# Kernel tuning notes

Measured on AMD Instinct MI355X. Metric: run time of the kernel, lower is better.

Reference implementation:

```python
import jax, jax.numpy as jnp
import numpy as np

N = 8192
IN_F = 256
OUT_F = 64
ALPHA = 0.2
NEG_INF = -9e15


def setup_inputs() -> dict:
    key = jax.random.key(0)
    k1, k2, k3, k4 = jax.random.split(key, 4)
    h = jax.random.normal(k1, (N, IN_F), dtype=jnp.float32)
    W = jax.random.normal(k2, (IN_F, OUT_F), dtype=jnp.float32) * (1.414 / np.sqrt(IN_F))
    a = jax.random.normal(k3, (2 * OUT_F, 1), dtype=jnp.float32) * (1.414 / np.sqrt(2 * OUT_F))
    adj = jax.random.randint(k4, (N, N), 0, 2, dtype=jnp.int32)
    return {"h": h, "W": W, "a": a, "adj": adj}


def reference(h, W, a, adj):
    # Wh: [N, F]
    Wh = h @ W
    # Decompose concat-based attention: e_ij = LeakyReLU(Wh_i . a[:F] + Wh_j . a[F:])
    a1, a2 = a[:OUT_F], a[OUT_F:]
    src = Wh @ a1              # [N, 1] contribution of row i
    dst = Wh @ a2              # [N, 1] contribution of col j
    e = jax.nn.leaky_relu(src + dst.T, negative_slope=ALPHA)  # [N, N]
    e = jnp.where(adj > 0, e, NEG_INF)
    attention = jax.nn.softmax(e, axis=1)
    # dropout is identity in eval mode
    h_prime = attention @ Wh   # [N, F]
    return h_prime
```

## Files before the change

### kernel.cpp

```cpp
#include <hip/hip_runtime.h>

#define NROWS 8192
#define NSPLIT 16
#define JT (NROWS / NSPLIT)
#define NITER (JT / 64)
#define L2E 1.4426950408889634f

typedef __attribute__((ext_vector_type(4))) float f32x4;
typedef __attribute__((ext_vector_type(8))) __bf16 bf16x8;
typedef __attribute__((ext_vector_type(4))) unsigned int u32x4;

__device__ __forceinline__ unsigned short f2bf(float x) {
  unsigned u = __float_as_uint(x);
  u += 0x7fffu + ((u >> 16) & 1u);
  return (unsigned short)(u >> 16);
}

__global__ __launch_bounds__(256) void k_prep(
    const float* __restrict__ h, const float* __restrict__ W,
    const float* __restrict__ a, unsigned short* __restrict__ WhB,
    float* __restrict__ src, float* __restrict__ dst) {
  int i = blockIdx.x * 4 + (threadIdx.x >> 6);
  int lane = threadIdx.x & 63;
  const float* hrow = h + (size_t)i * 256;
  float s = 0.f;
#pragma unroll 4
  for (int k = 0; k < 256; k += 4) {
    float4 hv = *(const float4*)(hrow + k);
    s = fmaf(hv.x, W[(k + 0) * 64 + lane], s);
    s = fmaf(hv.y, W[(k + 1) * 64 + lane], s);
    s = fmaf(hv.z, W[(k + 2) * 64 + lane], s);
    s = fmaf(hv.w, W[(k + 3) * 64 + lane], s);
  }
  int nt = lane >> 4, c = lane & 15;
  int gi = (i >> 3) & 3, e = i & 7;
  int idx = ((((i >> 5) * 4 + nt) * 64) + c + 16 * gi) * 8 + e;
  WhB[idx] = f2bf(s);
  float v1 = s * a[lane];
  float v2 = s * a[64 + lane];
#pragma unroll
  for (int d = 32; d; d >>= 1) {
    v1 += __shfl_xor(v1, d);
    v2 += __shfl_xor(v2, d);
  }
  if (lane == 0) {
    src[i] = v1 * L2E;
    dst[i] = v2 * L2E;
  }
}

__global__ __launch_bounds__(256) void k_dmax(
    const float* __restrict__ dst, float* __restrict__ dmax) {
  __shared__ float red[4];
  float v = -INFINITY;
  for (int i = threadIdx.x; i < NROWS; i += 256) v = fmaxf(v, dst[i]);
#pragma unroll
  for (int d = 32; d; d >>= 1) v = fmaxf(v, __shfl_xor(v, d));
  if ((threadIdx.x & 63) == 0) red[threadIdx.x >> 6] = v;
  __syncthreads();
  if (threadIdx.x == 0)
    *dmax = fmaxf(fmaxf(red[0], red[1]), fmaxf(red[2], red[3]));
}

__global__ __launch_bounds__(256, 8) void k_attn(
    const int* __restrict__ adj, const unsigned short* __restrict__ WhB,
    const float* __restrict__ src, const float* __restrict__ dst,
    const float* __restrict__ dmax,
    float* __restrict__ pl, float* __restrict__ pacc) {
  __shared__ float ldst[JT];
  int task = blockIdx.x * 4 + (threadIdx.x >> 6);
  int sp = task >> 9;
  int mt = task & 511;
  int lane = threadIdx.x & 63;
  int r = lane & 15;
  int g = lane >> 4;
  int row0 = mt * 16;
  int jbase = sp * JT;

  for (int k = threadIdx.x; k < JT; k += 256) ldst[k] = dst[jbase + k];
  __syncthreads();

  unsigned long long mk0 = 0, mk1 = 0;
  {
    const int* abase = adj + (size_t)row0 * NROWS + jbase + lane;
#pragma unroll
    for (int rr = 0; rr < 16; ++rr) {
      const int* rp = abase + (size_t)rr * NROWS;
#pragma unroll
      for (int ch = 0; ch < 8; ++ch) {
        int v = rp[ch * 64];
        unsigned long long bal = __ballot(v > 0);
        const int holder = ((ch & 3) << 4) + rr;
        if (ch < 4) mk0 = (lane == holder) ? bal : mk0;
        else        mk1 = (lane == holder) ? bal : mk1;
      }
    }
  }

  float srcr = src[row0 + r];
  float vB = srcr + *dmax;
  float Mi = fmaxf(vB, 0.2f * vB);

  float lrow = 0.f;
  f32x4 acc[4] = {f32x4{0.f, 0.f, 0.f, 0.f}, f32x4{0.f, 0.f, 0.f, 0.f},
                  f32x4{0.f, 0.f, 0.f, 0.f}, f32x4{0.f, 0.f, 0.f, 0.f}};
  const bf16x8* Bfr = (const bf16x8*)WhB;

#define PE(P, BIT, DD)                    \
  {                                       \
    float v_ = srcr + (DD);               \
    v_ = fmaxf(v_, 0.2f * v_);            \
    float e_ = exp2f(v_ - Mi);            \
    (P) = (BIT) ? e_ : 0.f;               \
  }
#define HALF(JC, BITS, DOFF)                                               \
  {                                                                        \
    const bf16x8* bp = Bfr + (size_t)(JC) * 256 + lane;                    \
    bf16x8 b0 = bp[0];                                                     \
    bf16x8 b1 = bp[64];                                                    \
    bf16x8 b2 = bp[128];                                                   \
    bf16x8 b3 = bp[192];                                                   \
    const float4* dlp = (const float4*)(ldst + (DOFF));                    \
    float4 dA = dlp[0];                                                    \
    float4 dB = dlp[1];                                                    \
    unsigned bt_ = (BITS);                                                 \
    float p0, p1, p2, p3, p4, p5, p6, p7;                                  \
    PE(p0, bt_ & 1u, dA.x)   PE(p1, bt_ & 2u, dA.y)                        \
    PE(p2, bt_ & 4u, dA.z)   PE(p3, bt_ & 8u, dA.w)                        \
    PE(p4, bt_ & 16u, dB.x)  PE(p5, bt_ & 32u, dB.y)                       \
    PE(p6, bt_ & 64u, dB.z)  PE(p7, bt_ & 128u, dB.w)                      \
    lrow += ((p0 + p1) + (p2 + p3)) + ((p4 + p5) + (p6 + p7));             \
    unsigned q0, q1, q2, q3;                                               \
    asm("v_cvt_pk_bf16_f32 %0, %1, %2" : "=v"(q0) : "v"(p0), "v"(p1));     \
    asm("v_cvt_pk_bf16_f32 %0, %1, %2" : "=v"(q1) : "v"(p2), "v"(p3));     \
    asm("v_cvt_pk_bf16_f32 %0, %1, %2" : "=v"(q2) : "v"(p4), "v"(p5));     \
    asm("v_cvt_pk_bf16_f32 %0, %1, %2" : "=v"(q3) : "v"(p6), "v"(p7));     \
    u32x4 qv = {q0, q1, q2, q3};                                           \
    bf16x8 Af = __builtin_bit_cast(bf16x8, qv);                            \
    __builtin_amdgcn_s_setprio(1);                                         \
    acc[0] = __builtin_amdgcn_mfma_f32_16x16x32_bf16(Af, b0, acc[0], 0, 0, 0); \
    acc[1] = __builtin_amdgcn_mfma_f32_16x16x32_bf16(Af, b1, acc[1], 0, 0, 0); \
    acc[2] = __builtin_amdgcn_mfma_f32_16x16x32_bf16(Af, b2, acc[2], 0, 0, 0); \
    acc[3] = __builtin_amdgcn_mfma_f32_16x16x32_bf16(Af, b3, acc[3], 0, 0, 0); \
    __builtin_amdgcn_s_setprio(0);                                         \
  }

#pragma unroll 1
  for (int it = 0; it < NITER; ++it) {
    unsigned long long msrc = (it < 4) ? mk0 : mk1;
    unsigned long long pw = __shfl(msrc, ((it & 3) << 4) + r);
    int jc = sp * 16 + 2 * it;
    HALF(jc, (unsigned)(pw >> (8 * g)), it * 64 + 8 * g)
    HALF(jc + 1, (unsigned)(pw >> (32 + 8 * g)), it * 64 + 32 + 8 * g)
  }
#undef HALF
#undef PE

  lrow += __shfl_xor(lrow, 16);
  lrow += __shfl_xor(lrow, 32);
  if (lane < 16) pl[sp * NROWS + row0 + lane] = lrow;
#pragma unroll
  for (int nt = 0; nt < 4; nt++)
#pragma unroll
    for (int q2 = 0; q2 < 4; q2++)
      pacc[((size_t)sp * NROWS + row0 + 4 * g + q2) * 64 + nt * 16 + r] = acc[nt][q2];
}

__global__ __launch_bounds__(256) void k_comb(
    const float* __restrict__ pl, const float* __restrict__ pacc,
    float* __restrict__ out) {
  int t = blockIdx.x * 256 + threadIdx.x;
  int row = t >> 6, f = t & 63;
  float L = 0.f, o = 0.f;
#pragma unroll
  for (int s2 = 0; s2 < NSPLIT; s2++) {
    L += pl[s2 * NROWS + row];
    o += pacc[((size_t)s2 * NROWS + row) * 64 + f];
  }
  out[t] = o / L;
}

extern "C" void kernel_launch(void* const* d_in, const int* in_sizes, int n_in,
                              void* d_out, int out_size, void* d_ws, size_t ws_size,
                              hipStream_t stream) {
  const float* h = (const float*)d_in[0];
  const float* W = (const float*)d_in[1];
  const float* a = (const float*)d_in[2];
  const int* adj = (const int*)d_in[3];
  float* out = (float*)d_out;

  char* ws = (char*)d_ws;
  unsigned short* WhB = (unsigned short*)ws;
  float* src = (float*)(ws + 0x100000);
  float* dst = (float*)(ws + 0x108000);
  float* dmax = (float*)(ws + 0x110000);
  float* pl = (float*)(ws + 0x110100);
  float* pacc = (float*)(ws + 0x190100);

  hipLaunchKernelGGL(k_prep, dim3(NROWS / 4), dim3(256), 0, stream, h, W, a, WhB, src, dst);
  hipLaunchKernelGGL(k_dmax, dim3(1), dim3(256), 0, stream, dst, dmax);
  hipLaunchKernelGGL(k_attn, dim3(2048), dim3(256), 0, stream,
                     adj, WhB, src, dst, dmax, pl, pacc);
  hipLaunchKernelGGL(k_comb, dim3(NROWS * 64 / 256), dim3(256), 0, stream, pl, pacc, out);
}
```

Measured before the change: 132.8 us.

## Vectorize adjacency loads to int4 and reorder partial-accumulator layout for coalescing

The adjacency mask is now read as int4 per lane instead of one int per lane, giving four ballots per load. The column-to-bit mapping changes to match, and the attention loop's bit extraction is rewritten accordingly. The partial accumulators are stored in an MFMA-fragment-native layout so each lane writes contiguously, and the combine kernel reads that layout. Occupancy hint in launch bounds is lowered from 8 to 5 waves, which gives the compiler more registers at the cost of fewer resident waves.

```diff
diff --git a/kernel.cpp b/kernel.cpp
--- a/kernel.cpp
+++ b/kernel.cpp
@@ -62,7 +62,7 @@
     *dmax = fmaxf(fmaxf(red[0], red[1]), fmaxf(red[2], red[3]));
 }
 
-__global__ __launch_bounds__(256, 8) void k_attn(
+__global__ __launch_bounds__(256, 5) void k_attn(
     const int* __restrict__ adj, const unsigned short* __restrict__ WhB,
     const float* __restrict__ src, const float* __restrict__ dst,
     const float* __restrict__ dmax,
@@ -82,17 +82,28 @@
 
   unsigned long long mk0 = 0, mk1 = 0;
   {
-    const int* abase = adj + (size_t)row0 * NROWS + jbase + lane;
+    const int* abase = adj + (size_t)row0 * NROWS + jbase;
 #pragma unroll
     for (int rr = 0; rr < 16; ++rr) {
-      const int* rp = abase + (size_t)rr * NROWS;
-#pragma unroll
-      for (int ch = 0; ch < 8; ++ch) {
-        int v = rp[ch * 64];
-        unsigned long long bal = __ballot(v > 0);
-        const int holder = ((ch & 3) << 4) + rr;
-        if (ch < 4) mk0 = (lane == holder) ? bal : mk0;
-        else        mk1 = (lane == holder) ? bal : mk1;
+      const int4* rp = (const int4*)(abase + (size_t)rr * NROWS);
+#pragma unroll
+      for (int q = 0; q < 2; ++q) {
+        int4 v = rp[q * 64 + lane];
+        unsigned long long bx = __ballot(v.x > 0);
+        unsigned long long by = __ballot(v.y > 0);
+        unsigned long long bz = __ballot(v.z > 0);
+        unsigned long long bw = __ballot(v.w > 0);
+        if (q == 0) {
+          mk0 = (lane == 0 + rr) ? bx : mk0;
+          mk0 = (lane == 16 + rr) ? by : mk0;
+          mk0 = (lane == 32 + rr) ? bz : mk0;
+          mk0 = (lane == 48 + rr) ? bw : mk0;
+        } else {
+          mk1 = (lane == 0 + rr) ? bx : mk1;
+          mk1 = (lane == 16 + rr) ? by : mk1;
+          mk1 = (lane == 32 + rr) ? bz : mk1;
+          mk1 = (lane == 48 + rr) ? bw : mk1;
+        }
       }
     }
   }
@@ -113,7 +124,7 @@
     float e_ = exp2f(v_ - Mi);            \
     (P) = (BIT) ? e_ : 0.f;               \
   }
-#define HALF(JC, BITS, DOFF)                                               \
+#define HALF(JC, A0_, A1_, A2_, A3_, DOFF)                                 \
   {                                                                        \
     const bf16x8* bp = Bfr + (size_t)(JC) * 256 + lane;                    \
     bf16x8 b0 = bp[0];                                                     \
@@ -123,12 +134,13 @@
     const float4* dlp = (const float4*)(ldst + (DOFF));                    \
     float4 dA = dlp[0];                                                    \
     float4 dB = dlp[1];                                                    \
-    unsigned bt_ = (BITS);                                                 \
     float p0, p1, p2, p3, p4, p5, p6, p7;                                  \
-    PE(p0, bt_ & 1u, dA.x)   PE(p1, bt_ & 2u, dA.y)                        \
-    PE(p2, bt_ & 4u, dA.z)   PE(p3, bt_ & 8u, dA.w)                        \
-    PE(p4, bt_ & 16u, dB.x)  PE(p5, bt_ & 32u, dB.y)                       \
-    PE(p6, bt_ & 64u, dB.z)  PE(p7, bt_ & 128u, dB.w)                      \
+    PE(p0, (unsigned)(A0_)&1u, dA.x) PE(p1, (unsigned)(A1_)&1u, dA.y)      \
+    PE(p2, (unsigned)(A2_)&1u, dA.z) PE(p3, (unsigned)(A3_)&1u, dA.w)      \
+    PE(p4, (unsigned)((A0_) >> 1) & 1u, dB.x)                              \
+    PE(p5, (unsigned)((A1_) >> 1) & 1u, dB.y)                              \
+    PE(p6, (unsigned)((A2_) >> 1) & 1u, dB.z)                              \
+    PE(p7, (unsigned)((A3_) >> 1) & 1u, dB.w)                              \
     lrow += ((p0 + p1) + (p2 + p3)) + ((p4 + p5) + (p6 + p7));             \
     unsigned q0, q1, q2, q3;                                               \
     asm("v_cvt_pk_bf16_f32 %0, %1, %2" : "=v"(q0) : "v"(p0), "v"(p1));     \
@@ -147,11 +159,20 @@
 
 #pragma unroll 1
   for (int it = 0; it < NITER; ++it) {
-    unsigned long long msrc = (it < 4) ? mk0 : mk1;
-    unsigned long long pw = __shfl(msrc, ((it & 3) << 4) + r);
+    unsigned long long ms = (it < 4) ? mk0 : mk1;
+    unsigned long long pw0 = __shfl(ms, r);
+    unsigned long long pw1 = __shfl(ms, 16 + r);
+    unsigned long long pw2 = __shfl(ms, 32 + r);
+    unsigned long long pw3 = __shfl(ms, 48 + r);
+
+    int l0 = (it & 3) * 16;
+    int s = l0 + 2 * g;
+    unsigned long long a0 = pw0 >> s, a1 = pw1 >> s, a2 = pw2 >> s, a3 = pw3 >> s;
+    unsigned long long h0 = a0 >> 8, h1 = a1 >> 8, h2 = a2 >> 8, h3 = a3 >> 8;
+
     int jc = sp * 16 + 2 * it;
-    HALF(jc, (unsigned)(pw >> (8 * g)), it * 64 + 8 * g)
-    HALF(jc + 1, (unsigned)(pw >> (32 + 8 * g)), it * 64 + 32 + 8 * g)
+    HALF(jc, a0, a1, a2, a3, it * 64 + 8 * g)
+    HALF(jc + 1, h0, h1, h2, h3, it * 64 + 32 + 8 * g)
   }
 #undef HALF
 #undef PE
@@ -163,7 +184,7 @@
   for (int nt = 0; nt < 4; nt++)
 #pragma unroll
     for (int q2 = 0; q2 < 4; q2++)
-      pacc[((size_t)sp * NROWS + row0 + 4 * g + q2) * 64 + nt * 16 + r] = acc[nt][q2];
+      pacc[((((size_t)sp * 512 + mt) * 4 + nt) * 4 + q2) * 64 + lane] = acc[nt][q2];
 }
 
 __global__ __launch_bounds__(256) void k_comb(
@@ -171,11 +192,14 @@
     float* __restrict__ out) {
   int t = blockIdx.x * 256 + threadIdx.x;
   int row = t >> 6, f = t & 63;
+  int mt = row >> 4, rem = row & 15, g = rem >> 2, q = rem & 3;
+  int nt = f >> 4, r = f & 15;
+  size_t base = ((((size_t)mt) * 4 + nt) * 4 + q) * 64 + g * 16 + r;
   float L = 0.f, o = 0.f;
 #pragma unroll
   for (int s2 = 0; s2 < NSPLIT; s2++) {
     L += pl[s2 * NROWS + row];
-    o += pacc[((size_t)s2 * NROWS + row) * 64 + f];
+    o += pacc[(size_t)s2 * (512 * 4 * 4 * 64) + base];
   }
   out[t] = o / L;
 }
```

After: 127.4 us. -4.1%, faster.

## Pre-pack adjacency bitmask and factor exp of leaky-relu into per-row/col products

Applied to the files above, without the earlier changes.

Adds a separate kernel that streams the int32 adjacency matrix with int4 loads and packs it into 64-bit ballot masks laid out for the attention kernel's access pattern. The attention kernel no longer reads adj; it loads compact mask words. It also replaces the per-element exp2 of the leaky-relu with max(Ai*exp2(dj), Ci*exp2(0.2*dj)), using precomputed per-column exponentials in LDS and per-row factors. The pacc layout is changed to coalesced per-lane stores, with the combine kernel reindexed to match. Occupancy hint drops from 8 to 5, at the cost of an extra kernel launch and extra global traffic for the packed mask.

```diff
diff --git a/kernel.cpp b/kernel.cpp
--- a/kernel.cpp
+++ b/kernel.cpp
@@ -3,7 +3,6 @@
 #define NROWS 8192
 #define NSPLIT 16
 #define JT (NROWS / NSPLIT)
-#define NITER (JT / 64)
 #define L2E 1.4426950408889634f
 
 typedef __attribute__((ext_vector_type(4))) float f32x4;
@@ -62,12 +61,41 @@
     *dmax = fmaxf(fmaxf(red[0], red[1]), fmaxf(red[2], red[3]));
 }
 
-__global__ __launch_bounds__(256, 8) void k_attn(
-    const int* __restrict__ adj, const unsigned short* __restrict__ WhB,
+__global__ __launch_bounds__(256) void k_mask(
+    const int* __restrict__ adj, unsigned long long* __restrict__ packed) {
+  int w = blockIdx.x * 4 + (threadIdx.x >> 6);
+  int lane = threadIdx.x & 63;
+  int row = w >> 4;
+  int s0 = (w & 15) * 2;
+  const int4* rp = (const int4*)(adj + (size_t)row * NROWS);
+  int4 v0 = rp[s0 * 64 + lane];
+  int4 v1 = rp[s0 * 64 + 64 + lane];
+  unsigned long long b0 = __ballot(v0.x > 0);
+  unsigned long long b1 = __ballot(v0.y > 0);
+  unsigned long long b2 = __ballot(v0.z > 0);
+  unsigned long long b3 = __ballot(v0.w > 0);
+  unsigned long long b4 = __ballot(v1.x > 0);
+  unsigned long long b5 = __ballot(v1.y > 0);
+  unsigned long long b6 = __ballot(v1.z > 0);
+  unsigned long long b7 = __ballot(v1.w > 0);
+  if (lane < 8) {
+    int c = lane & 3;
+    int seg = s0 + (lane >> 2);
+    unsigned long long val = (lane == 0) ? b0 : (lane == 1) ? b1
+                           : (lane == 2) ? b2 : (lane == 3) ? b3
+                           : (lane == 4) ? b4 : (lane == 5) ? b5
+                           : (lane == 6) ? b6 : b7;
+    packed[((size_t)seg * NROWS + row) * 4 + c] = val;
+  }
+}
+
+__global__ __launch_bounds__(256, 5) void k_attn(
+    const unsigned long long* __restrict__ packed,
+    const unsigned short* __restrict__ WhB,
     const float* __restrict__ src, const float* __restrict__ dst,
     const float* __restrict__ dmax,
     float* __restrict__ pl, float* __restrict__ pacc) {
-  __shared__ float ldst[JT];
+  __shared__ float2 ldst2[JT];
   int task = blockIdx.x * 4 + (threadIdx.x >> 6);
   int sp = task >> 9;
   int mt = task & 511;
@@ -77,58 +105,42 @@
   int row0 = mt * 16;
   int jbase = sp * JT;
 
-  for (int k = threadIdx.x; k < JT; k += 256) ldst[k] = dst[jbase + k];
+  for (int k = threadIdx.x; k < JT; k += 256) {
+    float dj = dst[jbase + k];
+    ldst2[k] = make_float2(exp2f(dj), exp2f(0.2f * dj));
+  }
   __syncthreads();
-
-  unsigned long long mk0 = 0, mk1 = 0;
-  {
-    const int* abase = adj + (size_t)row0 * NROWS + jbase + lane;
-#pragma unroll
-    for (int rr = 0; rr < 16; ++rr) {
-      const int* rp = abase + (size_t)rr * NROWS;
-#pragma unroll
-      for (int ch = 0; ch < 8; ++ch) {
-        int v = rp[ch * 64];
-        unsigned long long bal = __ballot(v > 0);
-        const int holder = ((ch & 3) << 4) + rr;
-        if (ch < 4) mk0 = (lane == holder) ? bal : mk0;
-        else        mk1 = (lane == holder) ? bal : mk1;
-      }
-    }
-  }
 
   float srcr = src[row0 + r];
   float vB = srcr + *dmax;
   float Mi = fmaxf(vB, 0.2f * vB);
+  float Ai = exp2f(srcr - Mi);
+  float Ci = exp2f(0.2f * srcr - Mi);
 
   float lrow = 0.f;
   f32x4 acc[4] = {f32x4{0.f, 0.f, 0.f, 0.f}, f32x4{0.f, 0.f, 0.f, 0.f},
                   f32x4{0.f, 0.f, 0.f, 0.f}, f32x4{0.f, 0.f, 0.f, 0.f}};
   const bf16x8* Bfr = (const bf16x8*)WhB;
 
-#define PE(P, BIT, DD)                    \
-  {                                       \
-    float v_ = srcr + (DD);               \
-    v_ = fmaxf(v_, 0.2f * v_);            \
-    float e_ = exp2f(v_ - Mi);            \
-    (P) = (BIT) ? e_ : 0.f;               \
-  }
-#define HALF(JC, BITS, DOFF)                                               \
+#define PE(P, BIT, BV, DV)                         \
+  {                                                \
+    float e_ = fmaxf(Ai * (BV), Ci * (DV));        \
+    (P) = ((unsigned)(BIT)&1u) ? e_ : 0.f;         \
+  }
+#define HALF(JC, A0_, A1_, A2_, A3_, DOFF)                                 \
   {                                                                        \
     const bf16x8* bp = Bfr + (size_t)(JC) * 256 + lane;                    \
     bf16x8 b0 = bp[0];                                                     \
     bf16x8 b1 = bp[64];                                                    \
     bf16x8 b2 = bp[128];                                                   \
     bf16x8 b3 = bp[192];                                                   \
-    const float4* dlp = (const float4*)(ldst + (DOFF));                    \
-    float4 dA = dlp[0];                                                    \
-    float4 dB = dlp[1];                                                    \
-    unsigned bt_ = (BITS);                                                 \
+    const float4* dlp = (const float4*)(ldst2 + (DOFF));                   \
+    float4 d0 = dlp[0], d1 = dlp[1], d2 = dlp[2], d3 = dlp[3];             \
     float p0, p1, p2, p3, p4, p5, p6, p7;                                  \
-    PE(p0, bt_ & 1u, dA.x)   PE(p1, bt_ & 2u, dA.y)                        \
-    PE(p2, bt_ & 4u, dA.z)   PE(p3, bt_ & 8u, dA.w)                        \
-    PE(p4, bt_ & 16u, dB.x)  PE(p5, bt_ & 32u, dB.y)                       \
-    PE(p6, bt_ & 64u, dB.z)  PE(p7, bt_ & 128u, dB.w)                      \
+    PE(p0, (A0_), d0.x, d0.y)      PE(p1, (A1_), d0.z, d0.w)               \
+    PE(p2, (A2_), d1.x, d1.y)      PE(p3, (A3_), d1.z, d1.w)               \
+    PE(p4, (A0_) >> 1, d2.x, d2.y) PE(p5, (A1_) >> 1, d2.z, d2.w)          \
+    PE(p6, (A2_) >> 1, d3.x, d3.y) PE(p7, (A3_) >> 1, d3.z, d3.w)          \
     lrow += ((p0 + p1) + (p2 + p3)) + ((p4 + p5) + (p6 + p7));             \
     unsigned q0, q1, q2, q3;                                               \
     asm("v_cvt_pk_bf16_f32 %0, %1, %2" : "=v"(q0) : "v"(p0), "v"(p1));     \
@@ -146,12 +158,29 @@
   }
 
 #pragma unroll 1
-  for (int it = 0; it < NITER; ++it) {
-    unsigned long long msrc = (it < 4) ? mk0 : mk1;
-    unsigned long long pw = __shfl(msrc, ((it & 3) << 4) + r);
-    int jc = sp * 16 + 2 * it;
-    HALF(jc, (unsigned)(pw >> (8 * g)), it * 64 + 8 * g)
-    HALF(jc + 1, (unsigned)(pw >> (32 + 8 * g)), it * 64 + 32 + 8 * g)
+  for (int sg = 0; sg < 2; ++sg) {
+    int seg = sp * 2 + sg;
+    const ulonglong2* pwp =
+        (const ulonglong2*)(packed + ((size_t)seg * NROWS + row0 + r) * 4);
+    ulonglong2 wa = pwp[0];
+    ulonglong2 wb = pwp[1];
+    unsigned long long u0 = wa.x >> (2 * g);
+    unsigned long long u1 = wa.y >> (2 * g);
+    unsigned long long u2 = wb.x >> (2 * g);
+    unsigned long long u3 = wb.y >> (2 * g);
+#pragma unroll
+    for (int inner = 0; inner < 4; ++inner) {
+      int it = sg * 4 + inner;
+      int jb = it * 64;
+      unsigned long long a0 = u0 >> (inner * 16);
+      unsigned long long a1 = u1 >> (inner * 16);
+      unsigned long long a2 = u2 >> (inner * 16);
+      unsigned long long a3 = u3 >> (inner * 16);
+      unsigned long long h0 = a0 >> 8, h1 = a1 >> 8, h2 = a2 >> 8, h3 = a3 >> 8;
+      int jc = sp * 16 + 2 * it;
+      HALF(jc, a0, a1, a2, a3, jb + 8 * g)
+      HALF(jc + 1, h0, h1, h2, h3, jb + 32 + 8 * g)
+    }
   }
 #undef HALF
 #undef PE
@@ -163,7 +192,7 @@
   for (int nt = 0; nt < 4; nt++)
 #pragma unroll
     for (int q2 = 0; q2 < 4; q2++)
-      pacc[((size_t)sp * NROWS + row0 + 4 * g + q2) * 64 + nt * 16 + r] = acc[nt][q2];
+      pacc[((((size_t)sp * 512 + mt) * 4 + nt) * 4 + q2) * 64 + lane] = acc[nt][q2];
 }
 
 __global__ __launch_bounds__(256) void k_comb(
@@ -171,11 +200,14 @@
     float* __restrict__ out) {
   int t = blockIdx.x * 256 + threadIdx.x;
   int row = t >> 6, f = t & 63;
+  int mt = row >> 4, rem = row & 15, g = rem >> 2, q = rem & 3;
+  int nt = f >> 4, r = f & 15;
+  size_t base = ((((size_t)mt) * 4 + nt) * 4 + q) * 64 + g * 16 + r;
   float L = 0.f, o = 0.f;
 #pragma unroll
   for (int s2 = 0; s2 < NSPLIT; s2++) {
     L += pl[s2 * NROWS + row];
-    o += pacc[((size_t)s2 * NROWS + row) * 64 + f];
+    o += pacc[(size_t)s2 * (512 * 4 * 4 * 64) + base];
   }
   out[t] = o / L;
 }
@@ -196,10 +228,12 @@
   float* dmax = (float*)(ws + 0x110000);
   float* pl = (float*)(ws + 0x110100);
   float* pacc = (float*)(ws + 0x190100);
+  unsigned long long* packed = (unsigned long long*)(ws + 0x2200000);
 
   hipLaunchKernelGGL(k_prep, dim3(NROWS / 4), dim3(256), 0, stream, h, W, a, WhB, src, dst);
   hipLaunchKernelGGL(k_dmax, dim3(1), dim3(256), 0, stream, dst, dmax);
+  hipLaunchKernelGGL(k_mask, dim3(32768), dim3(256), 0, stream, adj, packed);
   hipLaunchKernelGGL(k_attn, dim3(2048), dim3(256), 0, stream,
-                     adj, WhB, src, dst, dmax, pl, pacc);
+                     packed, WhB, src, dst, dmax, pl, pacc);
   hipLaunchKernelGGL(k_comb, dim3(NROWS * 64 / 256), dim3(256), 0, stream, pl, pacc, out);
 }
```

Result: slower. 136.9 us (+3.1%).
